# Performance work log

Measured on AMD Instinct MI355X. Metric: run time of the kernel, lower is better.

Reference implementation:

```python
import jax, jax.numpy as jnp
import numpy as np

EMBED_DIM = 2048
NUM_HEADS = 16
NUM_KV_HEADS = 4
KEY_DIM = EMBED_DIM // NUM_HEADS  # 128
B, S = 2, 2048


def setup_inputs() -> dict:
    key = jax.random.key(0)
    ks = jax.random.split(key, 8)
    kv_dim = KEY_DIM * NUM_KV_HEADS
    sc_in = 1.0 / np.sqrt(EMBED_DIM)
    return {
        "query": jax.random.normal(ks[0], (B, S, EMBED_DIM), jnp.float32),
        "key": jax.random.normal(ks[1], (B, S, EMBED_DIM), jnp.float32),
        "value": jax.random.normal(ks[2], (B, S, EMBED_DIM), jnp.float32),
        "mask": jnp.ones((B, S), jnp.float32),
        "Wq": jax.random.normal(ks[3], (EMBED_DIM, EMBED_DIM), jnp.float32) * sc_in,
        "Wk": jax.random.normal(ks[4], (EMBED_DIM, kv_dim), jnp.float32) * sc_in,
        "Wv": jax.random.normal(ks[5], (EMBED_DIM, kv_dim), jnp.float32) * sc_in,
        "Wo": jax.random.normal(ks[6], (EMBED_DIM, EMBED_DIM), jnp.float32) * sc_in,
    }


def reference(query, key, value, mask, Wq, Wk, Wv, Wo):
    b, sq, _ = query.shape
    skv = key.shape[1]
    scale = 1.0 / float(KEY_DIM) ** 0.5
    # projections (no bias)
    q = (query @ Wq).reshape(b, sq, NUM_HEADS, KEY_DIM).transpose(0, 2, 1, 3)      # [B,H,Sq,D]
    k = (key @ Wk).reshape(b, skv, NUM_KV_HEADS, KEY_DIM).transpose(0, 2, 1, 3)    # [B,Hkv,Skv,D]
    v = (value @ Wv).reshape(b, skv, NUM_KV_HEADS, KEY_DIM).transpose(0, 2, 1, 3)  # [B,Hkv,Skv,D]
    n_rep = NUM_HEADS // NUM_KV_HEADS
    k_rep = jnp.repeat(k, n_rep, axis=1)  # [B,H,Skv,D]
    v_rep = jnp.repeat(v, n_rep, axis=1)  # [B,H,Skv,D]
    scores = jnp.einsum("bhqd,bhkd->bhqk", q, k_rep) * scale  # [B,H,Sq,Skv]
    scores = scores + (1.0 - mask[:, None, None, :].astype(scores.dtype)) * -1e9
    attn = jax.nn.softmax(scores, axis=-1)
    out = jnp.einsum("bhqk,bhkd->bhqd", attn, v_rep)  # [B,H,Sq,D]
    out = out.transpose(0, 2, 1, 3).reshape(b, sq, EMBED_DIM)
    return out @ Wo
```

## Files before the change

kernel.cpp:

```cpp
#include <hip/hip_runtime.h>
#include <hip/hip_bf16.h>

#define B_    2
#define S_    2048
#define E_    2048
#define H_    16
#define HKV_  4
#define D_    128
#define NTOK  4096
#define KVDIM 512

typedef __bf16 bf16x8 __attribute__((ext_vector_type(8)));
typedef __bf16 bf16x4 __attribute__((ext_vector_type(4)));
typedef float  f32x4  __attribute__((ext_vector_type(4)));

__device__ __forceinline__ void async_copy16(const void* g, void* l) {
  __builtin_amdgcn_global_load_lds(
      (const __attribute__((address_space(1))) unsigned int*)g,
      (__attribute__((address_space(3))) unsigned int*)l, 16, 0, 0);
}

__global__ __launch_bounds__(256) void transpose_all(
    const float* __restrict__ Wq, const float* __restrict__ Wk,
    const float* __restrict__ Wv, const float* __restrict__ Wo,
    __bf16* __restrict__ WTq, __bf16* __restrict__ WTk,
    __bf16* __restrict__ WTv, __bf16* __restrict__ WoT) {
  const float* in;
  __bf16* out;
  int C;
  switch (blockIdx.z) {
    case 0:  in = Wq; out = WTq; C = E_;   break;
    case 1:  in = Wk; out = WTk; C = KVDIM; break;
    case 2:  in = Wv; out = WTv; C = KVDIM; break;
    default: in = Wo; out = WoT; C = E_;   break;
  }
  const int c0 = blockIdx.x * 32;
  if (c0 >= C) return;
  const int r0 = blockIdx.y * 32;
  __shared__ float t[32][33];
  const int tr = threadIdx.x >> 3;
  const int tc = (threadIdx.x & 7) * 4;
  const float* ip = in + (size_t)(r0 + tr) * C + c0 + tc;
#pragma unroll
  for (int i = 0; i < 4; ++i) t[tr][tc + i] = ip[i];
  __syncthreads();
  __bf16* op = out + (size_t)(c0 + tr) * E_ + r0 + tc;
#pragma unroll
  for (int i = 0; i < 4; ++i) op[i] = (__bf16)t[tc + i][tr];
}

__global__ __launch_bounds__(256) void convert_q(const float* __restrict__ in,
                                                 __bf16* __restrict__ ob) {
  const size_t i = ((size_t)blockIdx.x * 256 + threadIdx.x) * 8;
  const f32x4 a0 = *(const f32x4*)(in + i);
  const f32x4 a1 = *(const f32x4*)(in + i + 4);
  bf16x8 v;
#pragma unroll
  for (int j = 0; j < 4; ++j) { v[j] = (__bf16)a0[j]; v[4 + j] = (__bf16)a1[j]; }
  *(bf16x8*)(ob + i) = v;
}

__global__ __launch_bounds__(512, 1) void gemm_pipe(
    const __bf16* __restrict__ A, const __bf16* __restrict__ Bt,
    float* __restrict__ Cf, __bf16* __restrict__ Cb, int M, int N, int K,
    int epi) {
  __shared__ __align__(16) __bf16 lds[2 * 24576];

  const int n0 = blockIdx.x * 256;
  const int m0 = blockIdx.y * 128;
  const int tid = threadIdx.x;
  const int w = tid >> 6;
  const int lane = tid & 63;
  const int quad = lane >> 4;
  const int l16 = lane & 15;
  const int wm = w >> 2;
  const int wn = w & 3;
  const int lr = lane >> 3;
  const int ls = lane & 7;

  const __bf16* pa[2];
  const __bf16* pb[4];
#pragma unroll
  for (int r = 0; r < 2; ++r) {
    const int row = r * 64 + w * 8 + lr;
    pa[r] = A + (size_t)(m0 + row) * K + ((ls ^ (row & 7)) * 8);
  }
#pragma unroll
  for (int r = 0; r < 4; ++r) {
    const int row = r * 64 + w * 8 + lr;
    pb[r] = Bt + (size_t)(n0 + row) * K + ((ls ^ (row & 7)) * 8);
  }

  auto stageA = [&](int bufi) {
    __bf16* base = lds + bufi * 24576;
#pragma unroll
    for (int r = 0; r < 2; ++r) {
      async_copy16(pa[r], base + (size_t)(r * 64 + w * 8) * 64);
      pa[r] += 64;
    }
  };
  auto stageB = [&](int bufi) {
    __bf16* base = lds + bufi * 24576 + 8192;
#pragma unroll
    for (int r = 0; r < 4; ++r) {
      async_copy16(pb[r], base + (size_t)(r * 64 + w * 8) * 64);
      pb[r] += 64;
    }
  };

  f32x4 acc[4][4] = {};
  const int NT = K >> 6;
  const int xr = l16 & 7;

  stageA(0);
  stageB(0);
  stageB(1);
  asm volatile("s_waitcnt vmcnt(4)" ::: "memory");
  __builtin_amdgcn_s_barrier();

  for (int t = 0; t < NT; ++t) {
    const __bf16* lA = lds + (t & 1) * 24576;
    const __bf16* lB = lA + 8192;

    bf16x8 af[2][2], bfr[4][2];
#pragma unroll
    for (int f = 0; f < 2; ++f) {
      const int rowb = (wm * 64 + f * 16 + l16) * 64;
#pragma unroll
      for (int ks = 0; ks < 2; ++ks)
        af[f][ks] = *(const bf16x8*)&lA[rowb + (((ks * 4 + quad) ^ xr) * 8)];
    }
#pragma unroll
    for (int g = 0; g < 4; ++g) {
      const int rowb = (wn * 64 + g * 16 + l16) * 64;
#pragma unroll
      for (int ks = 0; ks < 2; ++ks)
        bfr[g][ks] = *(const bf16x8*)&lB[rowb + (((ks * 4 + quad) ^ xr) * 8)];
    }
    if (t + 1 < NT) stageA((t + 1) & 1);
    __builtin_amdgcn_s_barrier();
    asm volatile("s_waitcnt lgkmcnt(0)" ::: "memory");
    __builtin_amdgcn_sched_barrier(0);
    __builtin_amdgcn_s_setprio(1);
#pragma unroll
    for (int f = 0; f < 2; ++f)
#pragma unroll
      for (int g = 0; g < 4; ++g) {
        acc[f][g] = __builtin_amdgcn_mfma_f32_16x16x32_bf16(af[f][0], bfr[g][0],
                                                            acc[f][g], 0, 0, 0);
        acc[f][g] = __builtin_amdgcn_mfma_f32_16x16x32_bf16(af[f][1], bfr[g][1],
                                                            acc[f][g], 0, 0, 0);
      }
    __builtin_amdgcn_s_setprio(0);
    __builtin_amdgcn_s_barrier();

    bf16x8 ah[2][2];
#pragma unroll
    for (int f = 0; f < 2; ++f) {
      const int rowb = (wm * 64 + (f + 2) * 16 + l16) * 64;
#pragma unroll
      for (int ks = 0; ks < 2; ++ks)
        ah[f][ks] = *(const bf16x8*)&lA[rowb + (((ks * 4 + quad) ^ xr) * 8)];
    }
    if (t + 2 < NT) stageB(t & 1);
    __builtin_amdgcn_s_barrier();
    asm volatile("s_waitcnt lgkmcnt(0)" ::: "memory");
    __builtin_amdgcn_sched_barrier(0);
    __builtin_amdgcn_s_setprio(1);
#pragma unroll
    for (int f = 0; f < 2; ++f)
#pragma unroll
      for (int g = 0; g < 4; ++g) {
        acc[f + 2][g] = __builtin_amdgcn_mfma_f32_16x16x32_bf16(
            ah[f][0], bfr[g][0], acc[f + 2][g], 0, 0, 0);
        acc[f + 2][g] = __builtin_amdgcn_mfma_f32_16x16x32_bf16(
            ah[f][1], bfr[g][1], acc[f + 2][g], 0, 0, 0);
      }
    __builtin_amdgcn_s_setprio(0);

    if (t + 2 < NT) {
      asm volatile("s_waitcnt vmcnt(4)" ::: "memory");
      __builtin_amdgcn_s_barrier();
    } else if (t + 1 < NT) {
      asm volatile("s_waitcnt vmcnt(0)" ::: "memory");
      __builtin_amdgcn_s_barrier();
    }
  }

#pragma unroll
  for (int f = 0; f < 4; ++f) {
#pragma unroll
    for (int g = 0; g < 4; ++g) {
#pragma unroll
      for (int r = 0; r < 4; ++r) {
        const int m = m0 + wm * 64 + f * 16 + quad * 4 + r;
        const int n = n0 + wn * 64 + g * 16 + l16;
        if (epi == 0) Cf[(size_t)m * N + n] = acc[f][g][r];
        else          Cb[(size_t)m * N + n] = (__bf16)acc[f][g][r];
      }
    }
  }
}

__global__ __launch_bounds__(256, 2) void gemm_kv(
    const float* __restrict__ key, const float* __restrict__ value,
    const __bf16* __restrict__ WTk, const __bf16* __restrict__ WTv,
    __bf16* __restrict__ Kp, __bf16* __restrict__ Vt) {
  __shared__ __align__(16) __bf16 As[128 * 32];
  __shared__ __align__(16) __bf16 Bs[128 * 32];

  const int bx = blockIdx.x;
  const float* A;
  const __bf16* Bt;
  int n0, epi;
  if (bx < 4) { A = key;   Bt = WTk; n0 = bx * 128;       epi = 0; }
  else        { A = value; Bt = WTv; n0 = (bx - 4) * 128; epi = 1; }
  const int m0 = blockIdx.y * 128;
  const int K = E_;
  const int N = KVDIM;

  const int tid = threadIdx.x;
  const int w = tid >> 6;
  const int lane = tid & 63;
  const int quad = lane >> 4;
  const int l16 = lane & 15;
  const int wr = w >> 1, wc = w & 1;
  const int brow = lane >> 2;
  const int bcol = (lane & 3) * 8;
  const int arow = lane >> 2;
  const int acol = (lane & 3) * 8;

  f32x4 acc[4][4] = {};

  for (int k0 = 0; k0 < K; k0 += 32) {
    __syncthreads();
#pragma unroll
    for (int c = 0; c < 2; ++c) {
      const int chunk = w * 2 + c;
      const int row = chunk * 16 + brow;
      async_copy16(Bt + (size_t)(n0 + row) * K + k0 + bcol, &Bs[chunk * 512]);
    }
#pragma unroll
    for (int s = 0; s < 2; ++s) {
      const int row = w * 32 + s * 16 + arow;
      const float* src = A + (size_t)(m0 + row) * K + k0 + acol;
      const f32x4 a0 = *(const f32x4*)src;
      const f32x4 a1 = *(const f32x4*)(src + 4);
      bf16x8 v;
#pragma unroll
      for (int j = 0; j < 4; ++j) { v[j] = (__bf16)a0[j]; v[4 + j] = (__bf16)a1[j]; }
      *(bf16x8*)&As[row * 32 + acol] = v;
    }
    __syncthreads();
    bf16x8 af[4], bfr[4];
#pragma unroll
    for (int i = 0; i < 4; ++i)
      af[i] = *(const bf16x8*)&As[(wr * 64 + i * 16 + l16) * 32 + quad * 8];
#pragma unroll
    for (int j = 0; j < 4; ++j)
      bfr[j] = *(const bf16x8*)&Bs[(wc * 64 + j * 16 + l16) * 32 + quad * 8];
#pragma unroll
    for (int i = 0; i < 4; ++i)
#pragma unroll
      for (int j = 0; j < 4; ++j)
        acc[i][j] = __builtin_amdgcn_mfma_f32_16x16x32_bf16(af[i], bfr[j],
                                                            acc[i][j], 0, 0, 0);
  }

#pragma unroll
  for (int i = 0; i < 4; ++i) {
#pragma unroll
    for (int j = 0; j < 4; ++j) {
#pragma unroll
      for (int r = 0; r < 4; ++r) {
        const int m = m0 + wr * 64 + i * 16 + quad * 4 + r;
        const int n = n0 + wc * 64 + j * 16 + l16;
        if (epi == 0) {
          Kp[(size_t)m * N + n] = (__bf16)acc[i][j][r];
        } else {
          const int b = m >> 11, s = m & (S_ - 1);
          Vt[((size_t)((b * HKV_ + (n >> 7)) * D_ + (n & (D_ - 1)))) * S_ + s] =
              (__bf16)acc[i][j][r];
        }
      }
    }
  }
}

__global__ __launch_bounds__(256, 2) void attn_kernel(
    const __bf16* __restrict__ Q, const __bf16* __restrict__ Kp,
    const __bf16* __restrict__ Vt, const float* __restrict__ mask,
    __bf16* __restrict__ Oa) {
  __shared__ __align__(16) __bf16 K_lds[64][136];
  __shared__ __align__(16) __bf16 V_lds[128][72];
  __shared__ __align__(16) __bf16 P_lds[4][32][72];

  const int tid = threadIdx.x;
  const int w = tid >> 6, lane = tid & 63, quad = lane >> 4, l16 = lane & 15;
  const int bh = blockIdx.y;
  const int b = bh >> 4, h = bh & 15, hkv = h >> 2;
  const int q0 = blockIdx.x * 128 + w * 32;

  const __bf16* qbase = Q + (size_t)(b * S_ + q0) * E_ + h * D_;
  bf16x8 qf[2][4];
#pragma unroll
  for (int m = 0; m < 2; ++m)
#pragma unroll
    for (int ks = 0; ks < 4; ++ks)
      qf[m][ks] = *(const bf16x8*)(qbase + (size_t)(m * 16 + l16) * E_ +
                                   ks * 32 + quad * 8);

  const __bf16* kbase = Kp + (size_t)(b * S_) * KVDIM + hkv * D_;
  const __bf16* vbase = Vt + (size_t)((b * HKV_ + hkv) * D_) * S_;
  const float* mbase = mask + b * S_;

  const int kr = w * 16 + (lane >> 4);
  const int kc = (lane & 15) * 8;
  const int vr = w * 32 + (lane >> 3);
  const int vc = (lane & 7) * 8;

  bf16x8 kreg[4], vreg[4];
  auto fetch = [&](int kt) {
#pragma unroll
    for (int i = 0; i < 4; ++i)
      kreg[i] = *(const bf16x8*)(kbase + (size_t)(kt + kr + i * 4) * KVDIM + kc);
#pragma unroll
    for (int i = 0; i < 4; ++i)
      vreg[i] = *(const bf16x8*)(vbase + (size_t)(vr + i * 8) * S_ + kt + vc);
  };

  f32x4 o[2][8] = {};
  f32x4 lsum[2] = {};
  const float scale = 0.08838834764831845f;

  fetch(0);

  for (int kt = 0; kt < S_; kt += 64) {
#pragma unroll
    for (int i = 0; i < 4; ++i)
      *(bf16x8*)&K_lds[kr + i * 4][kc] = kreg[i];
#pragma unroll
    for (int i = 0; i < 4; ++i)
      *(bf16x8*)&V_lds[vr + i * 8][vc] = vreg[i];
    __syncthreads();

    if (kt + 64 < S_) fetch(kt + 64);

    f32x4 s[2][4] = {};
    __builtin_amdgcn_s_setprio(1);
#pragma unroll
    for (int ks = 0; ks < 4; ++ks) {
#pragma unroll
      for (int n = 0; n < 4; ++n) {
        bf16x8 kf = *(const bf16x8*)&K_lds[n * 16 + l16][ks * 32 + quad * 8];
        s[0][n] = __builtin_amdgcn_mfma_f32_16x16x32_bf16(qf[0][ks], kf,
                                                          s[0][n], 0, 0, 0);
        s[1][n] = __builtin_amdgcn_mfma_f32_16x16x32_bf16(qf[1][ks], kf,
                                                          s[1][n], 0, 0, 0);
      }
    }
    __builtin_amdgcn_s_setprio(0);

    float bias[4];
#pragma unroll
    for (int n = 0; n < 4; ++n)
      bias[n] = (1.0f - mbase[kt + n * 16 + l16]) * -1e9f;
#pragma unroll
    for (int m = 0; m < 2; ++m) {
#pragma unroll
      for (int n = 0; n < 4; ++n) {
#pragma unroll
        for (int r = 0; r < 4; ++r) {
          const float p = __expf(s[m][n][r] * scale + bias[n]);
          lsum[m][r] += p;
          P_lds[w][m * 16 + quad * 4 + r][n * 16 + l16] = (__bf16)p;
        }
      }
    }

    __builtin_amdgcn_s_setprio(1);
#pragma unroll
    for (int ks2 = 0; ks2 < 2; ++ks2) {
      bf16x8 pa[2];
#pragma unroll
      for (int m = 0; m < 2; ++m)
        pa[m] = *(const bf16x8*)&P_lds[w][m * 16 + l16][ks2 * 32 + quad * 8];
#pragma unroll
      for (int dt = 0; dt < 8; ++dt) {
        bf16x8 vf = *(const bf16x8*)&V_lds[dt * 16 + l16][ks2 * 32 + quad * 8];
        o[0][dt] = __builtin_amdgcn_mfma_f32_16x16x32_bf16(pa[0], vf,
                                                           o[0][dt], 0, 0, 0);
        o[1][dt] = __builtin_amdgcn_mfma_f32_16x16x32_bf16(pa[1], vf,
                                                           o[1][dt], 0, 0, 0);
      }
    }
    __builtin_amdgcn_s_setprio(0);

    __syncthreads();
  }

  __bf16* obase = Oa + (size_t)(b * S_ + q0) * E_ + h * D_;
#pragma unroll
  for (int m = 0; m < 2; ++m) {
#pragma unroll
    for (int r = 0; r < 4; ++r) {
      float v = lsum[m][r];
#pragma unroll
      for (int off = 1; off < 16; off <<= 1) v += __shfl_xor(v, off);
      const float inv = 1.0f / v;
#pragma unroll
      for (int dt = 0; dt < 8; ++dt)
        obase[(size_t)(m * 16 + quad * 4 + r) * E_ + dt * 16 + l16] =
            (__bf16)(o[m][dt][r] * inv);
    }
  }
}

extern "C" void kernel_launch(void* const* d_in, const int* in_sizes, int n_in,
                              void* d_out, int out_size, void* d_ws,
                              size_t ws_size, hipStream_t stream) {
  const float* query = (const float*)d_in[0];
  const float* key   = (const float*)d_in[1];
  const float* value = (const float*)d_in[2];
  const float* mask  = (const float*)d_in[3];
  const float* Wq    = (const float*)d_in[4];
  const float* Wk    = (const float*)d_in[5];
  const float* Wv    = (const float*)d_in[6];
  const float* Wo    = (const float*)d_in[7];
  float* out = (float*)d_out;

  __bf16* ws   = (__bf16*)d_ws;
  __bf16* Qp   = ws;
  __bf16* Kp   = Qp + (size_t)NTOK * E_;
  __bf16* Vt   = Kp + (size_t)NTOK * KVDIM;
  __bf16* WoT  = Vt + (size_t)NTOK * KVDIM;
  __bf16* WTq  = WoT + (size_t)E_ * E_;
  __bf16* WTk  = WTq + (size_t)E_ * E_;
  __bf16* WTv  = WTk + (size_t)KVDIM * E_;
  __bf16* Attn = WTq;
  __bf16* qb   = (__bf16*)d_out;

  transpose_all<<<dim3(64, 64, 4), 256, 0, stream>>>(Wq, Wk, Wv, Wo,
                                                     WTq, WTk, WTv, WoT);
  convert_q<<<dim3(4096), 256, 0, stream>>>(query, qb);
  gemm_kv<<<dim3(8, 32), 256, 0, stream>>>(key, value, WTk, WTv, Kp, Vt);
  gemm_pipe<<<dim3(E_ / 256, NTOK / 128), 512, 0, stream>>>(
      qb, WTq, nullptr, Qp, NTOK, E_, E_, 1);
  attn_kernel<<<dim3(S_ / 128, B_ * H_), 256, 0, stream>>>(Qp, Kp, Vt, mask,
                                                           Attn);
  gemm_pipe<<<dim3(E_ / 256, NTOK / 128), 512, 0, stream>>>(
      Attn, WoT, out, nullptr, NTOK, E_, E_, 0);
}
```

Before: 408.3 us.

## Vectorize weight transpose, prefetch mask with K/V, swizzle P tile in LDS

The weight transpose kernel now handles 64-row tiles, loading with 32-byte vector reads and storing 8 bf16 at once, which halves the grid and cuts scalar memory transactions. In the attention kernel, the mask values are prefetched into registers together with the next K/V tile, so their global-load latency no longer sits between the QK MFMAs and the softmax. The P tile written to LDS is XOR-swizzled on write and read to reduce bank conflicts. These changes add index arithmetic, and a mismatch between the write and read swizzle would corrupt results.

```diff
diff --git a/kernel.cpp b/kernel.cpp
--- a/kernel.cpp
+++ b/kernel.cpp
@@ -36,17 +36,24 @@
   }
   const int c0 = blockIdx.x * 32;
   if (c0 >= C) return;
-  const int r0 = blockIdx.y * 32;
-  __shared__ float t[32][33];
-  const int tr = threadIdx.x >> 3;
-  const int tc = (threadIdx.x & 7) * 4;
-  const float* ip = in + (size_t)(r0 + tr) * C + c0 + tc;
-#pragma unroll
-  for (int i = 0; i < 4; ++i) t[tr][tc + i] = ip[i];
+  const int r0 = blockIdx.y * 64;
+  __shared__ float t[32][65];
+  const int lr = threadIdx.x >> 2;
+  const int lc = (threadIdx.x & 3) * 8;
+  const float* ip = in + (size_t)(r0 + lr) * C + c0 + lc;
+  const f32x4 a0 = *(const f32x4*)ip;
+  const f32x4 a1 = *(const f32x4*)(ip + 4);
+#pragma unroll
+  for (int j = 0; j < 4; ++j) t[lc + j][lr] = a0[j];
+#pragma unroll
+  for (int j = 0; j < 4; ++j) t[lc + 4 + j][lr] = a1[j];
   __syncthreads();
-  __bf16* op = out + (size_t)(c0 + tr) * E_ + r0 + tc;
-#pragma unroll
-  for (int i = 0; i < 4; ++i) op[i] = (__bf16)t[tc + i][tr];
+  const int oc = threadIdx.x >> 3;
+  const int orr = (threadIdx.x & 7) * 8;
+  bf16x8 v;
+#pragma unroll
+  for (int j = 0; j < 8; ++j) v[j] = (__bf16)t[oc][orr + j];
+  *(bf16x8*)(out + (size_t)(c0 + oc) * E_ + r0 + orr) = v;
 }
 
 __global__ __launch_bounds__(256) void convert_q(const float* __restrict__ in,
@@ -318,8 +325,11 @@
   const int kc = (lane & 15) * 8;
   const int vr = w * 32 + (lane >> 3);
   const int vc = (lane & 7) * 8;
+  const int psw = (quad >> 1) << 5;
+  const int pks = l16 >> 3;
 
   bf16x8 kreg[4], vreg[4];
+  float mreg[4];
   auto fetch = [&](int kt) {
 #pragma unroll
     for (int i = 0; i < 4; ++i)
@@ -327,6 +337,9 @@
 #pragma unroll
     for (int i = 0; i < 4; ++i)
       vreg[i] = *(const bf16x8*)(vbase + (size_t)(vr + i * 8) * S_ + kt + vc);
+#pragma unroll
+    for (int n = 0; n < 4; ++n)
+      mreg[n] = mbase[kt + n * 16 + l16];
   };
 
   f32x4 o[2][8] = {};
@@ -342,6 +355,10 @@
 #pragma unroll
     for (int i = 0; i < 4; ++i)
       *(bf16x8*)&V_lds[vr + i * 8][vc] = vreg[i];
+    float bias[4];
+#pragma unroll
+    for (int n = 0; n < 4; ++n)
+      bias[n] = (1.0f - mreg[n]) * -1e9f;
     __syncthreads();
 
     if (kt + 64 < S_) fetch(kt + 64);
@@ -361,10 +378,6 @@
     }
     __builtin_amdgcn_s_setprio(0);
 
-    float bias[4];
-#pragma unroll
-    for (int n = 0; n < 4; ++n)
-      bias[n] = (1.0f - mbase[kt + n * 16 + l16]) * -1e9f;
 #pragma unroll
     for (int m = 0; m < 2; ++m) {
 #pragma unroll
@@ -373,7 +386,7 @@
         for (int r = 0; r < 4; ++r) {
           const float p = __expf(s[m][n][r] * scale + bias[n]);
           lsum[m][r] += p;
-          P_lds[w][m * 16 + quad * 4 + r][n * 16 + l16] = (__bf16)p;
+          P_lds[w][m * 16 + quad * 4 + r][(n * 16 + l16) ^ psw] = (__bf16)p;
         }
       }
     }
@@ -384,7 +397,8 @@
       bf16x8 pa[2];
 #pragma unroll
       for (int m = 0; m < 2; ++m)
-        pa[m] = *(const bf16x8*)&P_lds[w][m * 16 + l16][ks2 * 32 + quad * 8];
+        pa[m] = *(const bf16x8*)
+            &P_lds[w][m * 16 + l16][(ks2 ^ pks) * 32 + quad * 8];
 #pragma unroll
       for (int dt = 0; dt < 8; ++dt) {
         bf16x8 vf = *(const bf16x8*)&V_lds[dt * 16 + l16][ks2 * 32 + quad * 8];
@@ -440,7 +454,7 @@
   __bf16* Attn = WTq;
   __bf16* qb   = (__bf16*)d_out;
 
-  transpose_all<<<dim3(64, 64, 4), 256, 0, stream>>>(Wq, Wk, Wv, Wo,
+  transpose_all<<<dim3(64, 32, 4), 256, 0, stream>>>(Wq, Wk, Wv, Wo,
                                                      WTq, WTk, WTv, WoT);
   convert_q<<<dim3(4096), 256, 0, stream>>>(query, qb);
   gemm_kv<<<dim3(8, 32), 256, 0, stream>>>(key, value, WTk, WTv, Kp, Vt);
```

New measurement: 404.2 us. About the same (-1.0%).
